# Performance work log

Hardware: AMD Instinct MI355X
Metric: run time of the kernel (lower is better)

The kernel has to match this reference:

```python
import jax, jax.numpy as jnp
import numpy as np

NEG_BIG = 1e9  # large-negative bias used by the original TF code


def setup_inputs() -> dict:
    key = jax.random.key(0)
    kq, kk, kv = jax.random.split(key, 3)
    B, H, W, C, CV = 8, 64, 64, 128, 128
    return {
        "query": jax.random.normal(kq, (B, H, W, C), dtype=jnp.float32),
        "key": jax.random.normal(kk, (B, H, W, C), dtype=jnp.float32),
        "value": jax.random.normal(kv, (B, H, W, CV), dtype=jnp.float32),
    }


def reference(query, key, value):
    B, Hh, Ww, C = query.shape
    CV = value.shape[-1]
    Nq = Hh * Ww                      # canvas_size_q (flattened spatial)
    Nk = key.shape[1] * key.shape[2]  # canvas_size
    q = query.reshape(B, Nq, C)
    k = key.reshape(B, Nk, C)
    v = value.reshape(B, Nk, CV)
    # dense QK^T scores over the flattened canvas: [B, Nq, Nk]
    dot = jnp.einsum('bqc,bkc->bqk', q, k) / jnp.sqrt(jnp.asarray(C, dtype=q.dtype))
    # causal mask: 1 where key position j <= query position i (allowed)
    allowed = jnp.tril(jnp.ones((Nq, Nk), dtype=q.dtype))
    # softmax with large-negative bias on disallowed positions, then re-mask
    probs = jax.nn.softmax(dot - NEG_BIG * (1.0 - allowed), axis=-1) * allowed
    mixed = jnp.einsum('bqk,bkc->bqc', probs, v)
    return mixed.reshape(B, Hh, Ww, CV)
```

## Files before the change

### kernel.cpp

```cpp
#include <hip/hip_runtime.h>
#include <hip/hip_bf16.h>

typedef __bf16 bf16_t;
typedef __attribute__((ext_vector_type(8))) __bf16 bf16x8;
typedef __attribute__((ext_vector_type(4))) __bf16 bf16x4;
typedef __attribute__((ext_vector_type(4))) float floatx4;

static constexpr int NSEQ = 4096;
static constexpr int DIM  = 128;
static constexpr int BATCH = 8;
static constexpr size_t NELEM = (size_t)BATCH * NSEQ * DIM;
static constexpr size_t WS_NEED = 2 * NELEM * sizeof(bf16_t);

static constexpr int NSLOT_C = 80;
static constexpr int NSLOT_F = 144;
static constexpr size_t WS_COARSE =
    WS_NEED + (size_t)BATCH * NSLOT_C * (16384 + 128) * sizeof(float);
static constexpr size_t WS_FINE =
    WS_NEED + (size_t)BATCH * NSLOT_F * (16384 + 128) * sizeof(float);

static constexpr float SCALE_LOG2E = 0.08838834764831845f * 1.4426950408889634f;

__device__ __forceinline__ int slot_base_d(int qt, int lb) {
  int g = qt >> lb, r = qt & ((1 << lb) - 1);
  return (1 << lb) * ((g * (g + 1)) >> 1) + r * (g + 1);
}

__device__ __forceinline__ void gld16(bf16_t* l, const bf16_t* g) {
  __builtin_amdgcn_global_load_lds(
      (const __attribute__((address_space(1))) unsigned int*)g,
      (__attribute__((address_space(3))) unsigned int*)l, 16, 0, 0);
}

__device__ __forceinline__ bf16x8 ld8_f32s(const float* p, float s) {
  float4 a = *(const float4*)p;
  float4 b = *(const float4*)(p + 4);
  bf16x8 r = {(__bf16)(a.x * s), (__bf16)(a.y * s), (__bf16)(a.z * s), (__bf16)(a.w * s),
              (__bf16)(b.x * s), (__bf16)(b.y * s), (__bf16)(b.z * s), (__bf16)(b.w * s)};
  return r;
}


__global__ __launch_bounds__(256)
void prep_kernel(const float* __restrict__ K, const float* __restrict__ V,
                 bf16_t* __restrict__ Kb, bf16_t* __restrict__ Vt) {
  __shared__ bf16_t ldsT[128 * 66];
  const int bid = blockIdx.x;
  if (bid < 1536) {
    const size_t n4 = NELEM / 4;
    for (size_t i = (size_t)bid * 256 + threadIdx.x; i < n4; i += (size_t)1536 * 256) {
      float4 k = ((const float4*)K)[i];
      bf16x4 kv = {(__bf16)k.x, (__bf16)k.y, (__bf16)k.z, (__bf16)k.w};
      ((bf16x4*)Kb)[i] = kv;
    }
  } else {
    const int id = bid - 1536;
    const int b  = id & 7;
    const int kt = id >> 3;
    const float* src = V + ((size_t)(b * NSEQ + kt * 64)) * DIM;
    #pragma unroll
    for (int it = 0; it < 8; ++it) {
      const int idx = it * 256 + (int)threadIdx.x;
      const int k = idx >> 5, c4 = idx & 31;
      float4 v = ((const float4*)src)[idx];
      ldsT[(c4 * 4 + 0) * 66 + k] = (__bf16)v.x;
      ldsT[(c4 * 4 + 1) * 66 + k] = (__bf16)v.y;
      ldsT[(c4 * 4 + 2) * 66 + k] = (__bf16)v.z;
      ldsT[(c4 * 4 + 3) * 66 + k] = (__bf16)v.w;
    }
    __syncthreads();
    #pragma unroll
    for (int it = 0; it < 4; ++it) {
      const int task = it * 256 + (int)threadIdx.x;
      const int d = task >> 3, kg = task & 7;
      bf16x8 o;
      #pragma unroll
      for (int j = 0; j < 8; ++j) o[j] = ldsT[d * 66 + kg * 8 + j];
      *(bf16x8*)(Vt + ((size_t)b * DIM + d) * NSEQ + kt * 64 + kg * 8) = o;
    }
  }
}


template <bool MASK>
__device__ __forceinline__ void tile_compute_sw(
    const bf16_t* __restrict__ kbuf, const bf16_t* __restrict__ vbuf,
    const bf16x8 (&qf)[2][4], int l16, int quad, int wq32, int dd,
    floatx4 (&acc)[2][8], float (&lsum)[2]) {
  #pragma unroll
  for (int h = 0; h < 2; ++h) {
    float pr[2][8];
    #pragma unroll
    for (int cc = 0; cc < 2; ++cc) {
      const int c4 = 2 * h + cc;
      floatx4 s0 = {0.f, 0.f, 0.f, 0.f}, s1 = {0.f, 0.f, 0.f, 0.f};
      const bf16_t* krow = kbuf + (c4 * 16 + l16) * DIM;
      #pragma unroll
      for (int d = 0; d < 4; ++d) {
        bf16x8 kf = *(const bf16x8*)(krow + (((4 * d + quad) ^ l16) * 8));
        s0 = __builtin_amdgcn_mfma_f32_16x16x32_bf16(kf, qf[0][d], s0, 0, 0, 0);
        s1 = __builtin_amdgcn_mfma_f32_16x16x32_bf16(kf, qf[1][d], s1, 0, 0, 0);
      }
      #pragma unroll
      for (int r = 0; r < 4; ++r) {
        float v0 = s0[r], v1 = s1[r];
        if constexpr (MASK) {
          const int key = dd + 32 * h + 8 * quad + 4 * cc + r;
          v0 = (key <= wq32 + l16) ? v0 : -3.0e38f;
          v1 = (key <= wq32 + 16 + l16) ? v1 : -3.0e38f;
        }
        float p0 = __builtin_amdgcn_exp2f(v0);
        float p1 = __builtin_amdgcn_exp2f(v1);
        lsum[0] += p0; lsum[1] += p1;
        pr[0][4 * cc + r] = p0; pr[1][4 * cc + r] = p1;
      }
    }
    bf16x8 pf0, pf1;
    #pragma unroll
    for (int j = 0; j < 8; ++j) { pf0[j] = (__bf16)pr[0][j]; pf1[j] = (__bf16)pr[1][j]; }
    __builtin_amdgcn_s_setprio(1);
    #pragma unroll
    for (int c = 0; c < 8; ++c) {
      const bf16_t* vrow = vbuf + (c * 16 + l16) * 64;
      bf16x8 vf = *(const bf16x8*)(vrow + (((quad + 4 * h) ^ (l16 & 7)) * 8));
      acc[0][c] = __builtin_amdgcn_mfma_f32_16x16x32_bf16(pf0, vf, acc[0][c], 0, 0, 0);
      acc[1][c] = __builtin_amdgcn_mfma_f32_16x16x32_bf16(pf1, vf, acc[1][c], 0, 0, 0);
    }
    __builtin_amdgcn_s_setprio(0);
  }
}


__global__ __launch_bounds__(256, 2)
void causal_attn_splitk(const float* __restrict__ Qf, const bf16_t* __restrict__ Kb,
                        const bf16_t* __restrict__ Vt, float* __restrict__ Out,
                        float* __restrict__ Pp, float* __restrict__ Ls,
                        int lb, int nslot) {
  __shared__ __align__(16) bf16_t Kds[2][64 * DIM];
  __shared__ __align__(16) bf16_t Vds[2][DIM * 64];

  const int b = (int)blockIdx.x & 7;
  const int s = (nslot - 1) - ((int)blockIdx.x >> 3);
  int qt = 0, cch = 0;
  {
    const int bs = 1 << lb;
    int acc0 = 0;
    for (int g = 0; g < (32 >> lb); ++g) {
      const int bandw = bs * (g + 1);
      if (s < acc0 + bandw) {
        const int u = s - acc0;
        qt = g * bs + u / (g + 1);
        cch = u % (g + 1);
        break;
      }
      acc0 += bandw;
    }
  }
  const int ntot = 2 * qt + 2;
  const int nch  = (qt >> lb) + 1;
  const int nt_c = (ntot - 1 - cch) / nch + 1;

  const int tid  = (int)threadIdx.x;
  const int wave = tid >> 6;
  const int lane = tid & 63;
  const int l16  = lane & 15;
  const int quad = lane >> 4;
  const int wq32 = wave * 32;

  bf16x8 qf[2][4];
  #pragma unroll
  for (int m = 0; m < 2; ++m) {
    const float* qrow =
        Qf + ((size_t)b * NSEQ + qt * 128 + wq32 + m * 16 + l16) * DIM + quad * 8;
    #pragma unroll
    for (int d = 0; d < 4; ++d) qf[m][d] = ld8_f32s(qrow + 32 * d, SCALE_LOG2E);
  }

  const bf16_t* kg = Kb + (size_t)b * NSEQ * DIM;
  const bf16_t* vg = Vt + ((size_t)b * DIM + 32 * wave) * NSEQ;
  int koff[4], voff[4];
  #pragma unroll
  for (int i = 0; i < 4; ++i) {
    const int p    = 16 * wave + 4 * i + quad;
    const int srow = 32 * (wave >> 1) + 8 * i + 4 * (wave & 1) + quad;
    koff[i] = srow * DIM + ((l16 ^ (p & 15)) * 8);
    const int vrow = 8 * i + (lane >> 3);
    voff[i] = vrow * NSEQ + (((lane & 7) ^ (vrow & 7)) * 8);
  }

  floatx4 acc[2][8];
  #pragma unroll
  for (int m = 0; m < 2; ++m)
    #pragma unroll
    for (int c = 0; c < 8; ++c) acc[m][c] = (floatx4){0.f, 0.f, 0.f, 0.f};
  float lsum[2] = {0.f, 0.f};

  int nmask;
  if (nch == 1) nmask = 2;
  else nmask = (cch + (nt_c - 1) * nch >= ntot - 2) ? 1 : 0;
  const int nfull = nt_c - nmask;

  {
    const size_t kb0 = (size_t)cch * 64;
    bf16_t* kl = &Kds[0][wave * 2048];
    bf16_t* vl = &Vds[0][wave * 2048];
    #pragma unroll
    for (int i = 0; i < 4; ++i) {
      gld16(kl + i * 512, kg + kb0 * DIM + koff[i]);
      gld16(vl + i * 512, vg + kb0 + voff[i]);
    }
  }
  __syncthreads();

  int t = cch;
  for (int it = 0; it < nt_c; ++it) {
    const int cur = it & 1;
    if (it + 1 < nt_c) {
      const size_t kbn = (size_t)(t + nch) * 64;
      bf16_t* kl = &Kds[cur ^ 1][wave * 2048];
      bf16_t* vl = &Vds[cur ^ 1][wave * 2048];
      #pragma unroll
      for (int i = 0; i < 4; ++i) {
        gld16(kl + i * 512, kg + kbn * DIM + koff[i]);
        gld16(vl + i * 512, vg + kbn + voff[i]);
      }
    }
    __builtin_amdgcn_sched_barrier(0);
    if (it < nfull) {
      tile_compute_sw<false>(Kds[cur], Vds[cur], qf, l16, quad, wq32, 0, acc, lsum);
    } else {
      const int dd = (t - 2 * qt) * 64;
      if (dd + 63 <= wq32)
        tile_compute_sw<false>(Kds[cur], Vds[cur], qf, l16, quad, wq32, 0, acc, lsum);
      else if (wq32 + 31 >= dd)
        tile_compute_sw<true>(Kds[cur], Vds[cur], qf, l16, quad, wq32, dd, acc, lsum);
    }
    asm volatile("s_waitcnt vmcnt(0)" ::: "memory");
    __builtin_amdgcn_sched_barrier(0);
    __builtin_amdgcn_s_barrier();
    __builtin_amdgcn_sched_barrier(0);
    t += nch;
  }

  float lred[2];
  #pragma unroll
  for (int m = 0; m < 2; ++m) {
    float s2 = lsum[m];
    s2 += __shfl_xor(s2, 16, 64);
    s2 += __shfl_xor(s2, 32, 64);
    lred[m] = s2;
  }

  if (nch == 1) {
    #pragma unroll
    for (int m = 0; m < 2; ++m) {
      float invl[4];
      #pragma unroll
      for (int r = 0; r < 4; ++r)
        invl[r] = 1.0f / __shfl(lred[m], quad * 4 + r, 64);
      float* orow =
          Out + ((size_t)b * NSEQ + qt * 128 + wq32 + m * 16 + quad * 4) * DIM + l16;
      #pragma unroll
      for (int c = 0; c < 8; ++c)
        #pragma unroll
        for (int r = 0; r < 4; ++r)
          orow[(size_t)r * DIM + c * 16] = acc[m][c][r] * invl[r];
    }
  } else {
    const int slot = b * nslot + slot_base_d(qt, lb) + cch;
    #pragma unroll
    for (int m = 0; m < 2; ++m) {
      float* pb = Pp + (size_t)slot * 16384 +
                  ((size_t)(wq32 + m * 16 + quad * 4)) * 128 + l16;
      #pragma unroll
      for (int c = 0; c < 8; ++c)
        #pragma unroll
        for (int r = 0; r < 4; ++r)
          pb[(size_t)r * 128 + c * 16] = acc[m][c][r];
      if (quad == 0)
        Ls[(size_t)slot * 128 + wq32 + m * 16 + l16] = lred[m];
    }
  }
}


__global__ __launch_bounds__(256)
void combine_kernel(const float* __restrict__ Pp, const float* __restrict__ Ls,
                    float* __restrict__ Out, int lb, int nslot) {
  const int e    = (int)blockIdx.x >> 1;
  const int half = (int)blockIdx.x & 1;
  const int b    = e & 7;
  const int qt   = (1 << lb) + (e >> 3);
  const int s0   = b * nslot + slot_base_d(qt, lb);
  const int nch  = (qt >> lb) + 1;
  const int t = (int)threadIdx.x;
  #pragma unroll
  for (int j = 0; j < 8; ++j) {
    const int idx = j * 256 + t;
    const int q   = half * 64 + (idx >> 5);
    const int d4  = idx & 31;
    float4 v = {0.f, 0.f, 0.f, 0.f};
    float  l = 0.f;
    for (int ch = 0; ch < nch; ++ch) {
      const float* pc = Pp + (size_t)(s0 + ch) * 16384 + (size_t)q * 128 + d4 * 4;
      float4 a = *(const float4*)pc;
      v.x += a.x; v.y += a.y; v.z += a.z; v.w += a.w;
      l += Ls[(size_t)(s0 + ch) * 128 + q];
    }
    const float inv = 1.0f / l;
    float4 r = {v.x * inv, v.y * inv, v.z * inv, v.w * inv};
    *(float4*)(Out + ((size_t)b * NSEQ + qt * 128 + q) * DIM + d4 * 4) = r;
  }
}


template <bool MASK>
__device__ __forceinline__ void tile_compute(
    const bf16_t* __restrict__ kbuf, const bf16_t* __restrict__ vbuf,
    bf16_t* __restrict__ pl, const bf16x8 (&qf)[4],
    int l16, int quad, int wq, floatx4 (&acc)[8], float (&lsum)[4]) {
  floatx4 s[4];
  #pragma unroll
  for (int c4 = 0; c4 < 4; ++c4) s[c4] = (floatx4){0.f, 0.f, 0.f, 0.f};
  #pragma unroll
  for (int c4 = 0; c4 < 4; ++c4) {
    const bf16_t* krow = kbuf + (c4 * 16 + l16) * DIM;
    #pragma unroll
    for (int d = 0; d < 4; ++d) {
      bf16x8 kf = *(const bf16x8*)(krow + (((4 * d + quad) ^ l16) * 8));
      s[c4] = __builtin_amdgcn_mfma_f32_16x16x32_bf16(qf[d], kf, s[c4], 0, 0, 0);
    }
  }
  #pragma unroll
  for (int c4 = 0; c4 < 4; ++c4) {
    #pragma unroll
    for (int r = 0; r < 4; ++r) {
      float v = s[c4][r];
      if constexpr (MASK)
        v = (c4 * 16 + l16 <= wq + quad * 4 + r) ? v : -3.0e38f;
      float p = __builtin_amdgcn_exp2f(v);
      lsum[r] += p;
      pl[(quad * 4 + r) * 72 + c4 * 16 + l16] = (__bf16)p;
    }
  }
  asm volatile("s_waitcnt lgkmcnt(0)" ::: "memory");
  bf16x8 pfA = *(const bf16x8*)(pl + l16 * 72 + quad * 8);
  bf16x8 pfB = *(const bf16x8*)(pl + l16 * 72 + 32 + quad * 8);
  #pragma unroll
  for (int c = 0; c < 8; ++c) {
    const bf16_t* vrow = vbuf + (c * 16 + l16) * 64;
    bf16x8 vfA = *(const bf16x8*)(vrow + ((quad ^ (l16 & 7)) * 8));
    bf16x8 vfB = *(const bf16x8*)(vrow + (((quad + 4) ^ (l16 & 7)) * 8));
    acc[c] = __builtin_amdgcn_mfma_f32_16x16x32_bf16(pfA, vfA, acc[c], 0, 0, 0);
    acc[c] = __builtin_amdgcn_mfma_f32_16x16x32_bf16(pfB, vfB, acc[c], 0, 0, 0);
  }
}

__global__ __launch_bounds__(256)
void causal_attn_kernel(const float* __restrict__ Qf, const bf16_t* __restrict__ Kb,
                        const bf16_t* __restrict__ Vt, float* __restrict__ Out) {
  __shared__ __align__(16) bf16_t Kbuf[64 * DIM];
  __shared__ __align__(16) bf16_t Vbuf[DIM * 64];
  __shared__ __align__(16) bf16_t Pbuf[4][16 * 72];

  const int half = blockIdx.x >> 8;
  const int idx  = blockIdx.x & 255;
  const int b    = idx & 7;
  const int q32  = idx >> 3;
  const int qt64 = half ? q32 : 63 - q32;

  const int tid  = (int)threadIdx.x;
  const int wave = tid >> 6;
  const int lane = tid & 63;
  const int l16  = lane & 15;
  const int quad = lane >> 4;
  const int wq   = wave * 16;

  bf16x8 qf[4];
  {
    const float* qrow = Qf + ((size_t)b * NSEQ + qt64 * 64 + wq + l16) * DIM + quad * 8;
    #pragma unroll
    for (int d = 0; d < 4; ++d) qf[d] = ld8_f32s(qrow + 32 * d, SCALE_LOG2E);
  }

  const bf16_t* kg0 = Kb + ((size_t)b * NSEQ + 16 * wave) * DIM;
  const bf16_t* vg0 = Vt + ((size_t)b * DIM + 32 * wave) * NSEQ;
  int koff[4], voff[4];
  #pragma unroll
  for (int i = 0; i < 4; ++i) {
    const int krow = 4 * i + (lane >> 4);
    koff[i] = krow * DIM + (((lane & 15) ^ (krow & 15)) * 8);
    const int vrow = 8 * i + (lane >> 3);
    voff[i] = vrow * NSEQ + (((lane & 7) ^ ((lane >> 3) & 7)) * 8);
  }
  bf16_t* kl = Kbuf + 16 * wave * DIM;
  bf16_t* vl = Vbuf + 32 * wave * 64;
  bf16_t* pl = Pbuf[wave];

  floatx4 acc[8];
  #pragma unroll
  for (int c = 0; c < 8; ++c) acc[c] = (floatx4){0.f, 0.f, 0.f, 0.f};
  float lsum[4] = {0.f, 0.f, 0.f, 0.f};

  const int nk = qt64 + 1;
  for (int kt = 0; kt < nk - 1; ++kt) {
    const int kb = kt * 64;
    #pragma unroll
    for (int i = 0; i < 4; ++i) gld16(kl + i * 512, kg0 + (size_t)kb * DIM + koff[i]);
    #pragma unroll
    for (int i = 0; i < 4; ++i) gld16(vl + i * 512, vg0 + kb + voff[i]);
    __syncthreads();
    tile_compute<false>(Kbuf, Vbuf, pl, qf, l16, quad, wq, acc, lsum);
    __syncthreads();
  }
  {
    const int kb = (nk - 1) * 64;
    #pragma unroll
    for (int i = 0; i < 4; ++i) gld16(kl + i * 512, kg0 + (size_t)kb * DIM + koff[i]);
    #pragma unroll
    for (int i = 0; i < 4; ++i) gld16(vl + i * 512, vg0 + kb + voff[i]);
    __syncthreads();
    tile_compute<true>(Kbuf, Vbuf, pl, qf, l16, quad, wq, acc, lsum);
  }

  float inv_l[4];
  #pragma unroll
  for (int r = 0; r < 4; ++r) {
    float s = lsum[r];
    #pragma unroll
    for (int off = 1; off < 16; off <<= 1) s += __shfl_xor(s, off, 64);
    inv_l[r] = 1.0f / s;
  }
  float* orow = Out + ((size_t)b * NSEQ + qt64 * 64 + wq + quad * 4) * DIM + l16;
  #pragma unroll
  for (int c = 0; c < 8; ++c) {
    #pragma unroll
    for (int r = 0; r < 4; ++r)
      orow[(size_t)r * DIM + c * 16] = acc[c][r] * inv_l[r];
  }
}


__global__ __launch_bounds__(256)
void causal_attn_fb(const float* __restrict__ Qf, const float* __restrict__ Kf,
                    const float* __restrict__ Vf, float* __restrict__ Out) {
  __shared__ bf16_t p_lds[4][16 * 72];
  const int bid = blockIdx.x, t = bid >> 3, b = bid & 7;
  const int tid = (int)threadIdx.x, wave = tid >> 6, lane = tid & 63;
  const int l16 = lane & 15, quad = lane >> 4;
  const int qtile = (wave < 2) ? t : (127 - t);
  const int q_base = qtile * 32 + (wave & 1) * 16;

  bf16x8 qf[4];
  const float* qrow = Qf + ((size_t)b * NSEQ + q_base + l16) * DIM + quad * 8;
  #pragma unroll
  for (int d = 0; d < 4; ++d) qf[d] = ld8_f32s(qrow + 32 * d, SCALE_LOG2E);

  floatx4 acc[8];
  #pragma unroll
  for (int c = 0; c < 8; ++c) acc[c] = (floatx4){0.f, 0.f, 0.f, 0.f};
  float lsum[4] = {0.f, 0.f, 0.f, 0.f};
  bf16_t* pl = p_lds[wave];
  const int ntiles = (q_base + 16 + 63) >> 6;

  for (int kt = 0; kt < ntiles; ++kt) {
    const int kb = kt * 64;
    floatx4 s[4];
    #pragma unroll
    for (int c4 = 0; c4 < 4; ++c4) s[c4] = (floatx4){0.f, 0.f, 0.f, 0.f};
    const float* kbase = Kf + ((size_t)b * NSEQ + kb + l16) * DIM + quad * 8;
    #pragma unroll
    for (int c4 = 0; c4 < 4; ++c4) {
      #pragma unroll
      for (int d = 0; d < 4; ++d) {
        bf16x8 kf = ld8_f32s(kbase + (size_t)c4 * 16 * DIM + 32 * d, 1.0f);
        s[c4] = __builtin_amdgcn_mfma_f32_16x16x32_bf16(qf[d], kf, s[c4], 0, 0, 0);
      }
    }
    #pragma unroll
    for (int c4 = 0; c4 < 4; ++c4) {
      #pragma unroll
      for (int r = 0; r < 4; ++r) {
        float v = s[c4][r];
        const int qi = q_base + quad * 4 + r;
        v = (kb + c4 * 16 + l16 <= qi) ? v : -3.0e38f;
        float p = __builtin_amdgcn_exp2f(v);
        lsum[r] += p;
        pl[(quad * 4 + r) * 72 + c4 * 16 + l16] = (__bf16)p;
      }
    }
    asm volatile("s_waitcnt lgkmcnt(0)" ::: "memory");
    bf16x8 pfA = *(const bf16x8*)(pl + l16 * 72 + quad * 8);
    bf16x8 pfB = *(const bf16x8*)(pl + l16 * 72 + 32 + quad * 8);
    const float* vb = Vf + ((size_t)b * NSEQ + kb) * DIM;
    #pragma unroll
    for (int c = 0; c < 8; ++c) {
      bf16x8 vfA, vfB;
      #pragma unroll
      for (int j = 0; j < 8; ++j) {
        vfA[j] = (__bf16)vb[(size_t)(quad * 8 + j) * DIM + c * 16 + l16];
        vfB[j] = (__bf16)vb[(size_t)(32 + quad * 8 + j) * DIM + c * 16 + l16];
      }
      acc[c] = __builtin_amdgcn_mfma_f32_16x16x32_bf16(pfA, vfA, acc[c], 0, 0, 0);
      acc[c] = __builtin_amdgcn_mfma_f32_16x16x32_bf16(pfB, vfB, acc[c], 0, 0, 0);
    }
  }
  float inv_l[4];
  #pragma unroll
  for (int r = 0; r < 4; ++r) {
    float s = lsum[r];
    #pragma unroll
    for (int off = 1; off < 16; off <<= 1) s += __shfl_xor(s, off, 64);
    inv_l[r] = 1.0f / s;
  }
  float* orow = Out + ((size_t)b * NSEQ + q_base + quad * 4) * DIM + l16;
  #pragma unroll
  for (int c = 0; c < 8; ++c) {
    #pragma unroll
    for (int r = 0; r < 4; ++r)
      orow[(size_t)r * DIM + c * 16] = acc[c][r] * inv_l[r];
  }
}

extern "C" void kernel_launch(void* const* d_in, const int* in_sizes, int n_in,
                              void* d_out, int out_size, void* d_ws, size_t ws_size,
                              hipStream_t stream) {
  const float* Q = (const float*)d_in[0];
  const float* K = (const float*)d_in[1];
  const float* V = (const float*)d_in[2];
  float* Out = (float*)d_out;
  (void)in_sizes; (void)n_in; (void)out_size;

  dim3 block(256);
  if (ws_size >= WS_COARSE) {
    const bool fine = (ws_size >= WS_FINE);
    const int lb = fine ? 2 : 3;
    const int nslot = fine ? NSLOT_F : NSLOT_C;
    bf16_t* Kb = (bf16_t*)d_ws;
    bf16_t* Vt = Kb + NELEM;
    float*  Pp = (float*)((char*)d_ws + WS_NEED);
    float*  Ls = Pp + (size_t)BATCH * nslot * 16384;
    prep_kernel<<<dim3(2048), block, 0, stream>>>(K, V, Kb, Vt);
    causal_attn_splitk<<<dim3(BATCH * nslot), block, 0, stream>>>(Q, Kb, Vt, Out, Pp, Ls,
                                                                  lb, nslot);
    combine_kernel<<<dim3(BATCH * (32 - (1 << lb)) * 2), block, 0, stream>>>(Pp, Ls, Out,
                                                                             lb, nslot);
  } else if (ws_size >= WS_NEED) {
    bf16_t* Kb = (bf16_t*)d_ws;
    bf16_t* Vt = Kb + NELEM;
    prep_kernel<<<dim3(2048), block, 0, stream>>>(K, V, Kb, Vt);
    causal_attn_kernel<<<dim3(512), block, 0, stream>>>(Q, Kb, Vt, Out);
  } else {
    causal_attn_fb<<<dim3(512), block, 0, stream>>>(Q, K, V, Out);
  }
}
```

Baseline: 168.6 us.

## Load K/V fragments directly from global memory instead of LDS double-buffering

Removes the LDS double-buffered K/V staging in the split-K attention kernel and has each lane load its MFMA operand fragments straight from global memory (L2/cache), with a periodic barrier every other tile to keep waves loosely aligned. Freeing LDS lets occupancy rise to 3 blocks per CU via launch bounds. It also drops the fine 144-slot split path and always uses the coarse 80-slot partitioning. The trade is redundant global/cache traffic across the four waves and possibly exposed load latency in exchange for no LDS round trips or full block syncs.

```diff
diff --git a/kernel.cpp b/kernel.cpp
--- a/kernel.cpp
+++ b/kernel.cpp
@@ -13,11 +13,8 @@
 static constexpr size_t WS_NEED = 2 * NELEM * sizeof(bf16_t);
 
 static constexpr int NSLOT_C = 80;
-static constexpr int NSLOT_F = 144;
 static constexpr size_t WS_COARSE =
     WS_NEED + (size_t)BATCH * NSLOT_C * (16384 + 128) * sizeof(float);
-static constexpr size_t WS_FINE =
-    WS_NEED + (size_t)BATCH * NSLOT_F * (16384 + 128) * sizeof(float);
 
 static constexpr float SCALE_LOG2E = 0.08838834764831845f * 1.4426950408889634f;
 
@@ -83,8 +80,8 @@
 
 
 template <bool MASK>
-__device__ __forceinline__ void tile_compute_sw(
-    const bf16_t* __restrict__ kbuf, const bf16_t* __restrict__ vbuf,
+__device__ __forceinline__ void tile_direct(
+    const bf16_t* __restrict__ kq, const bf16_t* __restrict__ vq,
     const bf16x8 (&qf)[2][4], int l16, int quad, int wq32, int dd,
     floatx4 (&acc)[2][8], float (&lsum)[2]) {
   #pragma unroll
@@ -92,12 +89,11 @@
     float pr[2][8];
     #pragma unroll
     for (int cc = 0; cc < 2; ++cc) {
-      const int c4 = 2 * h + cc;
       floatx4 s0 = {0.f, 0.f, 0.f, 0.f}, s1 = {0.f, 0.f, 0.f, 0.f};
-      const bf16_t* krow = kbuf + (c4 * 16 + l16) * DIM;
+      const bf16_t* kp = kq + (32 * h + 4 * cc) * DIM;
       #pragma unroll
       for (int d = 0; d < 4; ++d) {
-        bf16x8 kf = *(const bf16x8*)(krow + (((4 * d + quad) ^ l16) * 8));
+        bf16x8 kf = *(const bf16x8*)(kp + 32 * d);
         s0 = __builtin_amdgcn_mfma_f32_16x16x32_bf16(kf, qf[0][d], s0, 0, 0, 0);
         s1 = __builtin_amdgcn_mfma_f32_16x16x32_bf16(kf, qf[1][d], s1, 0, 0, 0);
       }
@@ -121,8 +117,7 @@
     __builtin_amdgcn_s_setprio(1);
     #pragma unroll
     for (int c = 0; c < 8; ++c) {
-      const bf16_t* vrow = vbuf + (c * 16 + l16) * 64;
-      bf16x8 vf = *(const bf16x8*)(vrow + (((quad + 4 * h) ^ (l16 & 7)) * 8));
+      bf16x8 vf = *(const bf16x8*)(vq + (size_t)c * 16 * NSEQ + 32 * h);
       acc[0][c] = __builtin_amdgcn_mfma_f32_16x16x32_bf16(pf0, vf, acc[0][c], 0, 0, 0);
       acc[1][c] = __builtin_amdgcn_mfma_f32_16x16x32_bf16(pf1, vf, acc[1][c], 0, 0, 0);
     }
@@ -131,14 +126,11 @@
 }
 
 
-__global__ __launch_bounds__(256, 2)
+__global__ __launch_bounds__(256, 3)
 void causal_attn_splitk(const float* __restrict__ Qf, const bf16_t* __restrict__ Kb,
                         const bf16_t* __restrict__ Vt, float* __restrict__ Out,
                         float* __restrict__ Pp, float* __restrict__ Ls,
                         int lb, int nslot) {
-  __shared__ __align__(16) bf16_t Kds[2][64 * DIM];
-  __shared__ __align__(16) bf16_t Vds[2][DIM * 64];
-
   const int b = (int)blockIdx.x & 7;
   const int s = (nslot - 1) - ((int)blockIdx.x >> 3);
   int qt = 0, cch = 0;
@@ -176,17 +168,9 @@
     for (int d = 0; d < 4; ++d) qf[m][d] = ld8_f32s(qrow + 32 * d, SCALE_LOG2E);
   }
 
-  const bf16_t* kg = Kb + (size_t)b * NSEQ * DIM;
-  const bf16_t* vg = Vt + ((size_t)b * DIM + 32 * wave) * NSEQ;
-  int koff[4], voff[4];
-  #pragma unroll
-  for (int i = 0; i < 4; ++i) {
-    const int p    = 16 * wave + 4 * i + quad;
-    const int srow = 32 * (wave >> 1) + 8 * i + 4 * (wave & 1) + quad;
-    koff[i] = srow * DIM + ((l16 ^ (p & 15)) * 8);
-    const int vrow = 8 * i + (lane >> 3);
-    voff[i] = vrow * NSEQ + (((lane & 7) ^ (vrow & 7)) * 8);
-  }
+  const int krow_lane = 8 * (l16 >> 2) + (l16 & 3);
+  const bf16_t* kq0 = Kb + ((size_t)b * NSEQ + krow_lane) * DIM + quad * 8;
+  const bf16_t* vq0 = Vt + ((size_t)b * DIM + l16) * NSEQ + 8 * quad;
 
   floatx4 acc[2][8];
   #pragma unroll
@@ -200,46 +184,20 @@
   else nmask = (cch + (nt_c - 1) * nch >= ntot - 2) ? 1 : 0;
   const int nfull = nt_c - nmask;
 
-  {
-    const size_t kb0 = (size_t)cch * 64;
-    bf16_t* kl = &Kds[0][wave * 2048];
-    bf16_t* vl = &Vds[0][wave * 2048];
-    #pragma unroll
-    for (int i = 0; i < 4; ++i) {
-      gld16(kl + i * 512, kg + kb0 * DIM + koff[i]);
-      gld16(vl + i * 512, vg + kb0 + voff[i]);
-    }
-  }
-  __syncthreads();
-
   int t = cch;
-  for (int it = 0; it < nt_c; ++it) {
-    const int cur = it & 1;
-    if (it + 1 < nt_c) {
-      const size_t kbn = (size_t)(t + nch) * 64;
-      bf16_t* kl = &Kds[cur ^ 1][wave * 2048];
-      bf16_t* vl = &Vds[cur ^ 1][wave * 2048];
-      #pragma unroll
-      for (int i = 0; i < 4; ++i) {
-        gld16(kl + i * 512, kg + kbn * DIM + koff[i]);
-        gld16(vl + i * 512, vg + kbn + voff[i]);
-      }
-    }
-    __builtin_amdgcn_sched_barrier(0);
+  for (int it = 0; it < nt_c; ++it, t += nch) {
+    const bf16_t* kq = kq0 + (size_t)t * 64 * DIM;
+    const bf16_t* vq = vq0 + (size_t)t * 64;
     if (it < nfull) {
-      tile_compute_sw<false>(Kds[cur], Vds[cur], qf, l16, quad, wq32, 0, acc, lsum);
+      tile_direct<false>(kq, vq, qf, l16, quad, wq32, 0, acc, lsum);
     } else {
       const int dd = (t - 2 * qt) * 64;
       if (dd + 63 <= wq32)
-        tile_compute_sw<false>(Kds[cur], Vds[cur], qf, l16, quad, wq32, 0, acc, lsum);
+        tile_direct<false>(kq, vq, qf, l16, quad, wq32, 0, acc, lsum);
       else if (wq32 + 31 >= dd)
-        tile_compute_sw<true>(Kds[cur], Vds[cur], qf, l16, quad, wq32, dd, acc, lsum);
-    }
-    asm volatile("s_waitcnt vmcnt(0)" ::: "memory");
-    __builtin_amdgcn_sched_barrier(0);
-    __builtin_amdgcn_s_barrier();
-    __builtin_amdgcn_sched_barrier(0);
-    t += nch;
+        tile_direct<true>(kq, vq, qf, l16, quad, wq32, dd, acc, lsum);
+    }
+    if (it & 1) __builtin_amdgcn_s_barrier();
   }
 
   float lred[2];
@@ -533,9 +491,8 @@
 
   dim3 block(256);
   if (ws_size >= WS_COARSE) {
-    const bool fine = (ws_size >= WS_FINE);
-    const int lb = fine ? 2 : 3;
-    const int nslot = fine ? NSLOT_F : NSLOT_C;
+    const int lb = 3;
+    const int nslot = NSLOT_C;
     bf16_t* Kb = (bf16_t*)d_ws;
     bf16_t* Vt = Kb + NELEM;
     float*  Pp = (float*)((char*)d_ws + WS_NEED);
```

After: 373.8 us. 122% more time.

## Single-buffer V tile to raise split-k occupancy; split combine across more blocks

Applied to the files above, without the earlier changes.

The V shared-memory tile in the split-k attention kernel goes from double to single buffering, cutting LDS per block so launch bounds can request three blocks per CU instead of two. The next V tile is now loaded only after the current tile's compute and a barrier, followed by a full vmcnt wait and a second barrier, so V loads are no longer overlapped with compute. Separately, the combine kernel now uses four blocks per query tile of 32 rows each instead of two blocks of 64 rows, for more parallelism. The tradeoff is exposed V load latency and an extra barrier per iteration in exchange for higher occupancy, plus possible register pressure from the tighter launch bound.

```diff
diff --git a/kernel.cpp b/kernel.cpp
--- a/kernel.cpp
+++ b/kernel.cpp
@@ -131,13 +131,13 @@
 }
 
 
-__global__ __launch_bounds__(256, 2)
+__global__ __launch_bounds__(256, 3)
 void causal_attn_splitk(const float* __restrict__ Qf, const bf16_t* __restrict__ Kb,
                         const bf16_t* __restrict__ Vt, float* __restrict__ Out,
                         float* __restrict__ Pp, float* __restrict__ Ls,
                         int lb, int nslot) {
   __shared__ __align__(16) bf16_t Kds[2][64 * DIM];
-  __shared__ __align__(16) bf16_t Vds[2][DIM * 64];
+  __shared__ __align__(16) bf16_t Vds[DIM * 64];
 
   const int b = (int)blockIdx.x & 7;
   const int s = (nslot - 1) - ((int)blockIdx.x >> 3);
@@ -203,7 +203,7 @@
   {
     const size_t kb0 = (size_t)cch * 64;
     bf16_t* kl = &Kds[0][wave * 2048];
-    bf16_t* vl = &Vds[0][wave * 2048];
+    bf16_t* vl = &Vds[wave * 2048];
     #pragma unroll
     for (int i = 0; i < 4; ++i) {
       gld16(kl + i * 512, kg + kb0 * DIM + koff[i]);
@@ -213,33 +213,35 @@
   __syncthreads();
 
   int t = cch;
-  for (int it = 0; it < nt_c; ++it) {
+  for (int it = 0; it < nt_c; ++it, t += nch) {
     const int cur = it & 1;
-    if (it + 1 < nt_c) {
-      const size_t kbn = (size_t)(t + nch) * 64;
+    const bool more = (it + 1 < nt_c);
+    const size_t kbn = (size_t)(t + nch) * 64;
+    if (more) {
       bf16_t* kl = &Kds[cur ^ 1][wave * 2048];
-      bf16_t* vl = &Vds[cur ^ 1][wave * 2048];
-      #pragma unroll
-      for (int i = 0; i < 4; ++i) {
-        gld16(kl + i * 512, kg + kbn * DIM + koff[i]);
-        gld16(vl + i * 512, vg + kbn + voff[i]);
-      }
+      #pragma unroll
+      for (int i = 0; i < 4; ++i) gld16(kl + i * 512, kg + kbn * DIM + koff[i]);
     }
     __builtin_amdgcn_sched_barrier(0);
     if (it < nfull) {
-      tile_compute_sw<false>(Kds[cur], Vds[cur], qf, l16, quad, wq32, 0, acc, lsum);
+      tile_compute_sw<false>(Kds[cur], Vds, qf, l16, quad, wq32, 0, acc, lsum);
     } else {
       const int dd = (t - 2 * qt) * 64;
       if (dd + 63 <= wq32)
-        tile_compute_sw<false>(Kds[cur], Vds[cur], qf, l16, quad, wq32, 0, acc, lsum);
+        tile_compute_sw<false>(Kds[cur], Vds, qf, l16, quad, wq32, 0, acc, lsum);
       else if (wq32 + 31 >= dd)
-        tile_compute_sw<true>(Kds[cur], Vds[cur], qf, l16, quad, wq32, dd, acc, lsum);
-    }
-    asm volatile("s_waitcnt vmcnt(0)" ::: "memory");
+        tile_compute_sw<true>(Kds[cur], Vds, qf, l16, quad, wq32, dd, acc, lsum);
+    }
     __builtin_amdgcn_sched_barrier(0);
     __builtin_amdgcn_s_barrier();
-    __builtin_amdgcn_sched_barrier(0);
-    t += nch;
+    if (more) {
+      bf16_t* vl = &Vds[wave * 2048];
+      #pragma unroll
+      for (int i = 0; i < 4; ++i) gld16(vl + i * 512, vg + kbn + voff[i]);
+      asm volatile("s_waitcnt vmcnt(0)" ::: "memory");
+      __builtin_amdgcn_sched_barrier(0);
+      __builtin_amdgcn_s_barrier();
+    }
   }
 
   float lred[2];
@@ -287,17 +289,17 @@
 __global__ __launch_bounds__(256)
 void combine_kernel(const float* __restrict__ Pp, const float* __restrict__ Ls,
                     float* __restrict__ Out, int lb, int nslot) {
-  const int e    = (int)blockIdx.x >> 1;
-  const int half = (int)blockIdx.x & 1;
+  const int e    = (int)blockIdx.x >> 2;
+  const int qsub = (int)blockIdx.x & 3;
   const int b    = e & 7;
   const int qt   = (1 << lb) + (e >> 3);
   const int s0   = b * nslot + slot_base_d(qt, lb);
   const int nch  = (qt >> lb) + 1;
   const int t = (int)threadIdx.x;
   #pragma unroll
-  for (int j = 0; j < 8; ++j) {
+  for (int j = 0; j < 4; ++j) {
     const int idx = j * 256 + t;
-    const int q   = half * 64 + (idx >> 5);
+    const int q   = qsub * 32 + (idx >> 5);
     const int d4  = idx & 31;
     float4 v = {0.f, 0.f, 0.f, 0.f};
     float  l = 0.f;
@@ -543,7 +545,7 @@
     prep_kernel<<<dim3(2048), block, 0, stream>>>(K, V, Kb, Vt);
     causal_attn_splitk<<<dim3(BATCH * nslot), block, 0, stream>>>(Q, Kb, Vt, Out, Pp, Ls,
                                                                   lb, nslot);
-    combine_kernel<<<dim3(BATCH * (32 - (1 << lb)) * 2), block, 0, stream>>>(Pp, Ls, Out,
+    combine_kernel<<<dim3(BATCH * (32 - (1 << lb)) * 4), block, 0, stream>>>(Pp, Ls, Out,
                                                                              lb, nslot);
   } else if (ws_size >= WS_NEED) {
     bf16_t* Kb = (bf16_t*)d_ws;
```

Result: slower. 278.4 us (+65.1%).
